# Optimization experiments

Hardware: AMD Instinct MI355X
Metric: run time of the kernel (lower is better)

## Reference

```python
import jax, jax.numpy as jnp
import numpy as np

B, C, H, W = 8, 512, 64, 64
RED = 4
CR = C // RED  # 128

def setup_inputs() -> dict:
    key = jax.random.key(0)
    k1, k2, k3 = jax.random.split(key, 3)
    x = jax.random.normal(k1, (B, C, H, W), dtype=jnp.float32)
    # conv_in: 1x1 conv, no bias -> weight [3*CR, C]
    w_in = jax.random.normal(k2, (3 * CR, C), dtype=jnp.float32) * 0.02
    # conv_out: 1x1 conv, no bias -> weight [C, CR]
    w_out = jax.random.normal(k3, (C, CR), dtype=jnp.float32) * 0.02
    return {"x": x, "w_in": w_in, "w_out": w_out}

def reference(x, w_in, w_out):
    b, c, h, w = x.shape
    n = h * w
    xf = x.reshape(b, c, n)                         # flatten spatial -> [B,C,N]
    proj = jnp.einsum('oc,bcn->bon', w_in, xf)      # 1x1 conv_in -> [B,3*CR,N]
    emb_a, emb_b, g = jnp.split(proj, 3, axis=1)    # each [B,CR,N]
    # unscaled full self-attention over N spatial tokens
    weights = jnp.einsum('bcn,bcm->bnm', emb_a, emb_b)   # [B,N,N]
    weights = jax.nn.softmax(weights, axis=2)
    y = jnp.einsum('bnm,bcm->bnc', weights, g)           # [B,N,CR]
    y = jnp.einsum('oc,bnc->bon', w_out, y)              # 1x1 conv_out -> [B,C,N]
    return x + y.reshape(b, c, h, w)
```

## Files before the change

kernel.cpp:

```cpp
#include <hip/hip_runtime.h>


typedef __attribute__((ext_vector_type(8))) short short8;
typedef __attribute__((ext_vector_type(4))) float f32x4;
typedef __attribute__((ext_vector_type(16))) float f32x16;

__device__ inline unsigned bfr(float f) {
  union { float f; unsigned u; } v; v.f = f;
  return v.u + 0x8000u;
}
__device__ inline unsigned short f2bf(float f) { return (unsigned short)(bfr(f) >> 16); }
__device__ inline unsigned pack2(float a, float b) {
  return __builtin_amdgcn_perm(bfr(b), bfr(a), 0x07060302u);
}
__device__ inline int sw(int row, int col, int stride_halves) {
  return row * stride_halves + ((((col >> 3) ^ (row & 7)) << 3) | (col & 7));
}
__device__ inline void load_lds16(const void* g, void* l) {
  __builtin_amdgcn_global_load_lds(
      (const __attribute__((address_space(1))) unsigned int*)g,
      (__attribute__((address_space(3))) unsigned int*)l, 16, 0, 0);
}

__global__ __launch_bounds__(256) void k_prep(const float* __restrict__ w_in,
                                              const float* __restrict__ w_out,
                                              unsigned short* __restrict__ wi,
                                              unsigned short* __restrict__ wo) {
  int i = blockIdx.x * 256 + threadIdx.x;
  const float* src;
  unsigned short* dst;
  int base;
  if (i < 24576) { src = w_in;  dst = wi; base = i * 8; }
  else           { src = w_out; dst = wo; base = (i - 24576) * 8; }
  float4 d0 = *(const float4*)&src[base];
  float4 d1 = *(const float4*)&src[base + 4];
  uint4 p;
  p.x = pack2(d0.x, d0.y); p.y = pack2(d0.z, d0.w);
  p.z = pack2(d1.x, d1.y); p.w = pack2(d1.z, d1.w);
  *(uint4*)&dst[base] = p;
}

__global__ __launch_bounds__(256) void k_proj(const float* __restrict__ x,
                                              const unsigned short* __restrict__ wi,
                                              unsigned short* __restrict__ ab,
                                              unsigned short* __restrict__ gC) {
  __shared__ unsigned short A_lds[128 * 64];
  __shared__ unsigned short B_lds[64 * 64];
  const int t = threadIdx.x;
  const int lane = t & 63;
  const int w = t >> 6;
  const int l15 = lane & 15;
  const int quad = lane >> 4;
  const int n0 = blockIdx.x * 64;
  const int o0 = blockIdx.y * 128;
  const int b = blockIdx.z;
  const int ch8g = t >> 5;
  const int tp = t & 31;

  f32x4 acc[2][4];
#pragma unroll
  for (int i = 0; i < 2; i++)
#pragma unroll
    for (int j = 0; j < 4; j++) acc[i][j] = (f32x4)0.f;

  for (int k0 = 0; k0 < 512; k0 += 64) {
#pragma unroll
    for (int j = 0; j < 4; j++) {
      int row = w * 32 + j * 8 + (lane >> 3);
      int gs = (lane & 7) ^ (row & 7);
      load_lds16(&wi[(size_t)(o0 + row) * 512 + k0 + gs * 8],
                 (void*)&A_lds[(w * 32 + j * 8) * 64]);
    }
    {
      float2 d[8];
#pragma unroll
      for (int j = 0; j < 8; j++)
        d[j] = *(const float2*)&x[((size_t)(b * 512 + k0 + ch8g * 8 + j)) * 4096 + n0 + tp * 2];
#pragma unroll
      for (int i = 0; i < 2; i++) {
        int r = tp * 2 + i;
        uint4 pv;
        if (i == 0) {
          pv.x = pack2(d[0].x, d[1].x); pv.y = pack2(d[2].x, d[3].x);
          pv.z = pack2(d[4].x, d[5].x); pv.w = pack2(d[6].x, d[7].x);
        } else {
          pv.x = pack2(d[0].y, d[1].y); pv.y = pack2(d[2].y, d[3].y);
          pv.z = pack2(d[4].y, d[5].y); pv.w = pack2(d[6].y, d[7].y);
        }
        *(uint4*)&B_lds[sw(r, ch8g * 8, 64)] = pv;
      }
    }
    __syncthreads();
#pragma unroll
    for (int kk = 0; kk < 64; kk += 32) {
      short8 a0 = *(const short8*)&A_lds[sw(w * 32 + l15, kk + quad * 8, 64)];
      short8 a1 = *(const short8*)&A_lds[sw(w * 32 + 16 + l15, kk + quad * 8, 64)];
#pragma unroll
      for (int ns = 0; ns < 4; ns++) {
        short8 bb = *(const short8*)&B_lds[sw(ns * 16 + l15, kk + quad * 8, 64)];
        acc[0][ns] = __builtin_amdgcn_mfma_f32_16x16x32_bf16(a0, bb, acc[0][ns], 0, 0, 0);
        acc[1][ns] = __builtin_amdgcn_mfma_f32_16x16x32_bf16(a1, bb, acc[1][ns], 0, 0, 0);
      }
    }
    __syncthreads();
  }
  if (o0 < 256) {
#pragma unroll
    for (int ms = 0; ms < 2; ms++) {
      int o = o0 + w * 32 + ms * 16 + quad * 4;
#pragma unroll
      for (int ns = 0; ns < 4; ns++) {
        int n = n0 + ns * 16 + l15;
        uint2 p;
        p.x = pack2(acc[ms][ns][0], acc[ms][ns][1]);
        p.y = pack2(acc[ms][ns][2], acc[ms][ns][3]);
        *(uint2*)&ab[((size_t)(b * 4096 + n)) * 256 + o] = p;
      }
    }
  } else {
#pragma unroll
    for (int ms = 0; ms < 2; ms++) {
      int og = w * 32 + ms * 16 + quad * 4;
#pragma unroll
      for (int ns = 0; ns < 4; ns++) {
        int n = n0 + ns * 16 + l15;
#pragma unroll
        for (int r = 0; r < 4; r++)
          gC[((size_t)(b * 128 + og + r)) * 4096 + n] = f2bf(acc[ms][ns][r]);
      }
    }
  }
}

__global__ __launch_bounds__(256, 2) void k_attn(const unsigned short* __restrict__ ab,
                                                 const unsigned short* __restrict__ gC,
                                                 unsigned short* __restrict__ yt) {
  __shared__ uint4 smem4[65536 / 16];
  unsigned short* smem_h = (unsigned short*)smem4;
  float* Obuf = (float*)smem4;
  float* lsumbuf = (float*)((char*)smem4 + 33024);
  unsigned* Pbuf = (unsigned*)((char*)smem4 + 33280);

  const int t = threadIdx.x;
  const int lane = t & 63;
  const int w = t >> 6;
  const int wr = w & 1;
  const int wc = w >> 1;
  const int l31 = lane & 31;
  const int h = lane >> 5;
  const int l7 = l31 & 7;
  const int q0 = blockIdx.x * 64;
  const int b = blockIdx.y;

  short8 qf[8];
  {
    const unsigned short* qp = &ab[((size_t)(b * 4096 + q0 + wc * 32 + l31)) * 256 + h * 8];
#pragma unroll
    for (int ks = 0; ks < 8; ks++) qf[ks] = *(const short8*)&qp[ks * 16];
  }

  const int krow_c = w * 16 + (lane >> 4);
  const int vrow_c = w * 32 + (lane >> 3);

  auto dma_tile = [&](int kt, int buf) {
    unsigned short* Kb = smem_h + buf * 8192;
    unsigned short* Vb = smem_h + 16384 + buf * 8192;
#pragma unroll
    for (int j = 0; j < 4; j++) {
      int row = krow_c + j * 4;
      int gs = (lane & 15) ^ (row & 7);
      load_lds16(&ab[((size_t)(b * 4096 + kt + row)) * 256 + 128 + gs * 8],
                 (void*)&Kb[(w * 16 + j * 4) * 128]);
    }
#pragma unroll
    for (int j = 0; j < 4; j++) {
      int row = vrow_c + j * 8;
      int gs = (lane & 7) ^ (row & 7);
      load_lds16(&gC[((size_t)(b * 128 + row)) * 4096 + kt + gs * 8],
                 (void*)&Vb[(w * 32 + j * 8) * 64]);
    }
  };

  f32x16 O[4];
#pragma unroll
  for (int i = 0; i < 4; i++) O[i] = (f32x16)0.f;
  float lsum = 0.f;
  const int rowK = wr * 32 + l31;

  dma_tile(0, 0);
  __syncthreads();

  for (int it = 0; it < 64; ++it) {
    if (it < 63) dma_tile((it + 1) * 64, (it + 1) & 1);
    const unsigned short* Kc = smem_h + (it & 1) * 8192;
    const unsigned short* Vc = smem_h + 16384 + (it & 1) * 8192;

    f32x16 accS = (f32x16)0.f;
#pragma unroll
    for (int ks = 0; ks < 8; ks++) {
      short8 ak = *(const short8*)&Kc[rowK * 128 + (((ks * 2 + h) ^ l7) << 3)];
      accS = __builtin_amdgcn_mfma_f32_32x32x16_bf16(ak, qf[ks], accS, 0, 0, 0);
    }

    float ps[16];
#pragma unroll
    for (int r = 0; r < 16; r++) {
      ps[r] = __expf(accS[r]);
      lsum += ps[r];
    }
    unsigned u[8];
#pragma unroll
    for (int i = 0; i < 8; i++) u[i] = pack2(ps[2 * i], ps[2 * i + 1]);

    short8 pfrag[2];
#pragma unroll
    for (int f = 0; f < 2; f++) {
      unsigned a0 = u[4 * f + 0], a1 = u[4 * f + 1], a2 = u[4 * f + 2], a3 = u[4 * f + 3];
      unsigned r0 = __shfl_xor(h ? a0 : a2, 32);
      unsigned r1 = __shfl_xor(h ? a1 : a3, 32);
      union { unsigned uu[4]; short8 s; } cv;
      if (h == 0) { cv.uu[0] = a0; cv.uu[1] = a1; cv.uu[2] = r0; cv.uu[3] = r1; }
      else        { cv.uu[0] = r0; cv.uu[1] = r1; cv.uu[2] = a2; cv.uu[3] = a3; }
      pfrag[f] = cv.s;
    }

#pragma unroll
    for (int ct = 0; ct < 4; ct++) {
      int rowV = ct * 32 + l31;
#pragma unroll
      for (int f = 0; f < 2; f++) {
        short8 av = *(const short8*)&Vc[rowV * 64 + (((wr * 4 + f * 2 + h) ^ l7) << 3)];
        O[ct] = __builtin_amdgcn_mfma_f32_32x32x16_bf16(av, pfrag[f], O[ct], 0, 0, 0);
      }
    }
    __syncthreads();
  }

  lsum += __shfl_xor(lsum, 32);
  const int q = wc * 32 + l31;
  if (wr == 0) {
#pragma unroll
    for (int ct = 0; ct < 4; ct++)
#pragma unroll
      for (int r = 0; r < 16; r++) {
        int c = ct * 32 + (r & 3) + 8 * (r >> 2) + 4 * h;
        Obuf[q * 129 + c] = O[ct][r];
      }
    if (h == 0) lsumbuf[q] = lsum;
  }
  __syncthreads();
  if (wr == 1) {
    float linv = 1.f / (lsum + lsumbuf[q]);
#pragma unroll
    for (int ct = 0; ct < 4; ct++)
#pragma unroll
      for (int r = 0; r < 16; r += 2) {
        int c = ct * 32 + (r & 3) + 8 * (r >> 2) + 4 * h;
        float v0 = (Obuf[q * 129 + c] + O[ct][r]) * linv;
        float v1 = (Obuf[q * 129 + c + 1] + O[ct][r + 1]) * linv;
        Pbuf[q * 65 + (c >> 1)] = pack2(v0, v1);
      }
  }
  __syncthreads();
  {
    int qq = t >> 2, seg = t & 3;
    unsigned* yrow = (unsigned*)&yt[((size_t)(b * 4096 + q0 + qq)) * 128];
#pragma unroll
    for (int i = 0; i < 4; i++) {
      uint4 v;
      v.x = Pbuf[qq * 65 + seg * 16 + i * 4 + 0];
      v.y = Pbuf[qq * 65 + seg * 16 + i * 4 + 1];
      v.z = Pbuf[qq * 65 + seg * 16 + i * 4 + 2];
      v.w = Pbuf[qq * 65 + seg * 16 + i * 4 + 3];
      *(uint4*)&yrow[seg * 16 + i * 4] = v;
    }
  }
}

__global__ __launch_bounds__(256) void k_out(const float* __restrict__ x,
                                             const unsigned short* __restrict__ wo,
                                             const unsigned short* __restrict__ yt,
                                             float* __restrict__ out) {
  __shared__ unsigned short A_lds[128 * 128];
  __shared__ unsigned short B_lds[64 * 128];
  const int t = threadIdx.x;
  const int lane = t & 63;
  const int w = t >> 6;
  const int l15 = lane & 15;
  const int quad = lane >> 4;
  const int n0 = blockIdx.x * 64;
  const int o0 = blockIdx.y * 128;
  const int b = blockIdx.z;

#pragma unroll
  for (int j = 0; j < 8; j++) {
    int row = w * 32 + j * 4 + (lane >> 4);
    int gs = (lane & 15) ^ (row & 7);
    load_lds16(&wo[(size_t)(o0 + row) * 128 + gs * 8],
               (void*)&A_lds[(w * 32 + j * 4) * 128]);
  }
#pragma unroll
  for (int j = 0; j < 4; j++) {
    int row = w * 16 + j * 4 + (lane >> 4);
    int gs = (lane & 15) ^ (row & 7);
    load_lds16(&yt[((size_t)(b * 4096 + n0 + row)) * 128 + gs * 8],
               (void*)&B_lds[(w * 16 + j * 4) * 128]);
  }
  __syncthreads();

  f32x4 acc[2][4];
#pragma unroll
  for (int i = 0; i < 2; i++)
#pragma unroll
    for (int j = 0; j < 4; j++) acc[i][j] = (f32x4)0.f;
#pragma unroll
  for (int ks = 0; ks < 4; ks++) {
    short8 a0 = *(const short8*)&A_lds[sw(w * 32 + l15, ks * 32 + quad * 8, 128)];
    short8 a1 = *(const short8*)&A_lds[sw(w * 32 + 16 + l15, ks * 32 + quad * 8, 128)];
#pragma unroll
    for (int ns = 0; ns < 4; ns++) {
      short8 bb = *(const short8*)&B_lds[sw(ns * 16 + l15, ks * 32 + quad * 8, 128)];
      acc[0][ns] = __builtin_amdgcn_mfma_f32_16x16x32_bf16(a0, bb, acc[0][ns], 0, 0, 0);
      acc[1][ns] = __builtin_amdgcn_mfma_f32_16x16x32_bf16(a1, bb, acc[1][ns], 0, 0, 0);
    }
  }
#pragma unroll
  for (int ms = 0; ms < 2; ms++) {
    int o = o0 + w * 32 + ms * 16 + quad * 4;
#pragma unroll
    for (int ns = 0; ns < 4; ns++) {
      int n = n0 + ns * 16 + l15;
#pragma unroll
      for (int r = 0; r < 4; r++) {
        size_t off = ((size_t)(b * 512 + o + r)) * 4096 + n;
        out[off] = x[off] + acc[ms][ns][r];
      }
    }
  }
}

extern "C" void kernel_launch(void* const* d_in, const int* in_sizes, int n_in,
                              void* d_out, int out_size, void* d_ws, size_t ws_size,
                              hipStream_t stream) {
  const float* x = (const float*)d_in[0];
  const float* w_in = (const float*)d_in[1];
  const float* w_out = (const float*)d_in[2];
  float* out = (float*)d_out;

  unsigned short* ab = (unsigned short*)d_ws;
  unsigned short* gC = ab + (size_t)8 * 4096 * 256;
  unsigned short* yt = gC + (size_t)8 * 128 * 4096;
  unsigned short* wi = yt + (size_t)8 * 4096 * 128;
  unsigned short* wo = wi + (size_t)384 * 512;

  k_prep<<<128, 256, 0, stream>>>(w_in, w_out, wi, wo);
  k_proj<<<dim3(64, 3, 8), 256, 0, stream>>>(x, wi, ab, gC);
  k_attn<<<dim3(64, 8), 256, 0, stream>>>(ab, gC, yt);
  k_out<<<dim3(64, 4, 8), 256, 0, stream>>>(x, wo, yt, out);
}
```

Measured before the change: 241.4 us.

## Fold log2e into query weights, use exp2, cvt_pk, permlane swap, setprio

```diff
diff --git a/kernel.cpp b/kernel.cpp
--- a/kernel.cpp
+++ b/kernel.cpp
@@ -4,6 +4,7 @@
 typedef __attribute__((ext_vector_type(8))) short short8;
 typedef __attribute__((ext_vector_type(4))) float f32x4;
 typedef __attribute__((ext_vector_type(16))) float f32x16;
+typedef __attribute__((ext_vector_type(2))) unsigned int uint2v;
 
 __device__ inline unsigned bfr(float f) {
   union { float f; unsigned u; } v; v.f = f;
@@ -12,6 +13,11 @@
 __device__ inline unsigned short f2bf(float f) { return (unsigned short)(bfr(f) >> 16); }
 __device__ inline unsigned pack2(float a, float b) {
   return __builtin_amdgcn_perm(bfr(b), bfr(a), 0x07060302u);
+}
+__device__ inline unsigned cvtpk(float a, float b) {
+  unsigned r;
+  asm("v_cvt_pk_bf16_f32 %0, %1, %2" : "=v"(r) : "v"(a), "v"(b));
+  return r;
 }
 __device__ inline int sw(int row, int col, int stride_halves) {
   return row * stride_halves + ((((col >> 3) ^ (row & 7)) << 3) | (col & 7));
@@ -30,10 +36,17 @@
   const float* src;
   unsigned short* dst;
   int base;
-  if (i < 24576) { src = w_in;  dst = wi; base = i * 8; }
-  else           { src = w_out; dst = wo; base = (i - 24576) * 8; }
+  float s = 1.0f;
+  if (i < 24576) {
+    src = w_in;  dst = wi; base = i * 8;
+    if (base < 128 * 512) s = 1.4426950408889634f;
+  } else {
+    src = w_out; dst = wo; base = (i - 24576) * 8;
+  }
   float4 d0 = *(const float4*)&src[base];
   float4 d1 = *(const float4*)&src[base + 4];
+  d0.x *= s; d0.y *= s; d0.z *= s; d0.w *= s;
+  d1.x *= s; d1.y *= s; d1.z *= s; d1.w *= s;
   uint4 p;
   p.x = pack2(d0.x, d0.y); p.y = pack2(d0.z, d0.w);
   p.z = pack2(d1.x, d1.y); p.w = pack2(d1.z, d1.w);
@@ -149,8 +162,8 @@
   const int l31 = lane & 31;
   const int h = lane >> 5;
   const int l7 = l31 & 7;
-  const int q0 = blockIdx.x * 64;
-  const int b = blockIdx.y;
+  const int b = blockIdx.x & 7;
+  const int q0 = (blockIdx.x >> 3) * 64;
 
   short8 qf[8];
   {
@@ -184,7 +197,7 @@
   f32x16 O[4];
 #pragma unroll
   for (int i = 0; i < 4; i++) O[i] = (f32x16)0.f;
-  float lsum = 0.f;
+  float ls0 = 0.f, ls1 = 0.f, ls2 = 0.f, ls3 = 0.f;
   const int rowK = wr * 32 + l31;
 
   dma_tile(0, 0);
@@ -196,34 +209,36 @@
     const unsigned short* Vc = smem_h + 16384 + (it & 1) * 8192;
 
     f32x16 accS = (f32x16)0.f;
+    __builtin_amdgcn_s_setprio(1);
 #pragma unroll
     for (int ks = 0; ks < 8; ks++) {
       short8 ak = *(const short8*)&Kc[rowK * 128 + (((ks * 2 + h) ^ l7) << 3)];
       accS = __builtin_amdgcn_mfma_f32_32x32x16_bf16(ak, qf[ks], accS, 0, 0, 0);
     }
+    __builtin_amdgcn_s_setprio(0);
 
     float ps[16];
 #pragma unroll
-    for (int r = 0; r < 16; r++) {
-      ps[r] = __expf(accS[r]);
-      lsum += ps[r];
-    }
+    for (int r = 0; r < 16; r++) ps[r] = __builtin_amdgcn_exp2f(accS[r]);
+    ls0 += ps[0] + ps[4];  ls1 += ps[1] + ps[5];
+    ls2 += ps[2] + ps[6];  ls3 += ps[3] + ps[7];
+    ls0 += ps[8] + ps[12]; ls1 += ps[9] + ps[13];
+    ls2 += ps[10] + ps[14]; ls3 += ps[11] + ps[15];
     unsigned u[8];
 #pragma unroll
-    for (int i = 0; i < 8; i++) u[i] = pack2(ps[2 * i], ps[2 * i + 1]);
+    for (int i = 0; i < 8; i++) u[i] = cvtpk(ps[2 * i], ps[2 * i + 1]);
 
     short8 pfrag[2];
 #pragma unroll
     for (int f = 0; f < 2; f++) {
-      unsigned a0 = u[4 * f + 0], a1 = u[4 * f + 1], a2 = u[4 * f + 2], a3 = u[4 * f + 3];
-      unsigned r0 = __shfl_xor(h ? a0 : a2, 32);
-      unsigned r1 = __shfl_xor(h ? a1 : a3, 32);
+      uint2v r02 = __builtin_amdgcn_permlane32_swap(u[4 * f + 0], u[4 * f + 2], false, false);
+      uint2v r13 = __builtin_amdgcn_permlane32_swap(u[4 * f + 1], u[4 * f + 3], false, false);
       union { unsigned uu[4]; short8 s; } cv;
-      if (h == 0) { cv.uu[0] = a0; cv.uu[1] = a1; cv.uu[2] = r0; cv.uu[3] = r1; }
-      else        { cv.uu[0] = r0; cv.uu[1] = r1; cv.uu[2] = a2; cv.uu[3] = a3; }
+      cv.uu[0] = r02[0]; cv.uu[1] = r13[0]; cv.uu[2] = r02[1]; cv.uu[3] = r13[1];
       pfrag[f] = cv.s;
     }
 
+    __builtin_amdgcn_s_setprio(1);
 #pragma unroll
     for (int ct = 0; ct < 4; ct++) {
       int rowV = ct * 32 + l31;
@@ -233,9 +248,11 @@
         O[ct] = __builtin_amdgcn_mfma_f32_32x32x16_bf16(av, pfrag[f], O[ct], 0, 0, 0);
       }
     }
+    __builtin_amdgcn_s_setprio(0);
     __syncthreads();
   }
 
+  float lsum = (ls0 + ls1) + (ls2 + ls3);
   lsum += __shfl_xor(lsum, 32);
   const int q = wc * 32 + l31;
   if (wr == 0) {
@@ -355,6 +372,6 @@
 
   k_prep<<<128, 256, 0, stream>>>(w_in, w_out, wi, wo);
   k_proj<<<dim3(64, 3, 8), 256, 0, stream>>>(x, wi, ab, gC);
-  k_attn<<<dim3(64, 8), 256, 0, stream>>>(ab, gC, yt);
+  k_attn<<<dim3(512), 256, 0, stream>>>(ab, gC, yt);
   k_out<<<dim3(64, 4, 8), 256, 0, stream>>>(x, wo, yt, out);
 }
```

Result: faster. 233.3 us (-3.4%).
